# Performance work log

Measured on AMD Instinct MI355X. Metric: run time of the kernel, lower is better.

Reference implementation:

```python
import jax, jax.numpy as jnp
import numpy as np

NEG_SLOPE = 0.2  # PyG GATConv default negative_slope
EPS = 1e-16


def gat_conv(x, src, dst, num_nodes, W, att_src, att_dst, bias, concat):
    """PyG-style GATConv (eval mode, no dropout). att_*: [H, C]."""
    H, C = att_src.shape
    h = (x @ W).reshape(num_nodes, H, C)                      # [N,H,C]
    a_s = jnp.einsum('nhc,hc->nh', h, att_src)                # [N,H]
    a_d = jnp.einsum('nhc,hc->nh', h, att_dst)                # [N,H]
    e = jax.nn.leaky_relu(a_s[src] + a_d[dst], NEG_SLOPE)     # [E,H]
    # segment softmax over edges grouped by destination node
    m = jax.lax.stop_gradient(jax.ops.segment_max(e, dst, num_segments=num_nodes))
    ex = jnp.exp(e - m[dst])
    denom = jax.ops.segment_sum(ex, dst, num_segments=num_nodes)
    alpha = ex / (denom[dst] + EPS)                           # [E,H]
    msg = h[src] * alpha[:, :, None]                          # [E,H,C]
    out = jax.ops.segment_sum(msg, dst, num_segments=num_nodes)  # [N,H,C]
    out = out.reshape(num_nodes, H * C) if concat else out.mean(axis=1)
    return out + bias


def setup_inputs() -> dict:
    key = jax.random.key(0)
    ks = jax.random.split(key, 12)
    N, E = 65536, 1310720
    IN, HID, OUT, HEADS = 768, 128, 2, 8
    C1 = HID // HEADS  # 16
    s = 0.05
    return {
        'x': jax.random.normal(ks[0], (N, IN), jnp.float32),
        'edge_index': jax.random.randint(ks[1], (2, E), 0, N, jnp.int64),
        'W1': jax.random.normal(ks[2], (IN, HEADS * C1), jnp.float32) * s,
        'att_src1': jax.random.normal(ks[3], (HEADS, C1), jnp.float32) * s,
        'att_dst1': jax.random.normal(ks[4], (HEADS, C1), jnp.float32) * s,
        'b1': jnp.zeros((HID,), jnp.float32),
        'Wp': jax.random.normal(ks[5], (IN, HID), jnp.float32) * s,
        'bp': jnp.zeros((HID,), jnp.float32),
        'W2': jax.random.normal(ks[6], (HID, OUT), jnp.float32) * s,
        'att_src2': jax.random.normal(ks[7], (1, OUT), jnp.float32) * s,
        'att_dst2': jax.random.normal(ks[8], (1, OUT), jnp.float32) * s,
        'b2': jnp.zeros((OUT,), jnp.float32),
    }


def reference(x, edge_index, W1, att_src1, att_dst1, b1, Wp, bp, W2, att_src2, att_dst2, b2):
    N = x.shape[0]
    loops = jnp.arange(N, dtype=edge_index.dtype)  # add_self_loops=True
    src = jnp.concatenate([edge_index[0], loops])
    dst = jnp.concatenate([edge_index[1], loops])
    # eval mode: dropout is identity
    h1 = gat_conv(x, src, dst, N, W1, att_src1, att_dst1, b1, concat=True)
    h = jax.nn.elu(h1 + x @ Wp + bp)  # residual projection + ELU
    return gat_conv(h, src, dst, N, W2, att_src2, att_dst2, b2, concat=False)
```

## Files before the change

kernel.cpp:

```cpp
#include <hip/hip_runtime.h>
#include <hip/hip_bf16.h>
#include <math.h>

#define NEG_SLOPE 0.2f

typedef __attribute__((ext_vector_type(8))) short short8;
typedef __attribute__((ext_vector_type(4))) float float4v;

__device__ __forceinline__ unsigned f2bf(float f) {
  unsigned u = __builtin_bit_cast(unsigned, f);
  return (u + 0x7fffu + ((u >> 16) & 1u)) >> 16;
}
__device__ __forceinline__ float bflo(unsigned u) {
  return __builtin_bit_cast(float, u << 16);
}
__device__ __forceinline__ float bfhi(unsigned u) {
  return __builtin_bit_cast(float, u & 0xffff0000u);
}

__global__ __launch_bounds__(256) void convert_w(const float* __restrict__ W1,
                                                 const float* __restrict__ Wp,
                                                 short* __restrict__ Wt) {
  int k = blockIdx.x;
  int c = threadIdx.x;
  float v = (c < 128) ? W1[k * 128 + c] : Wp[k * 128 + (c - 128)];
  Wt[(size_t)c * 768 + k] = (short)f2bf(v);
}

__global__ __launch_bounds__(256) void gemm_mfma(
    const float* __restrict__ x, const short* __restrict__ Wt,
    const float* __restrict__ att_src1, const float* __restrict__ att_dst1,
    float* __restrict__ proj, unsigned* __restrict__ h1bf,
    float* __restrict__ a_s1, float* __restrict__ a_d1) {
  __shared__ short As[128][40];
  __shared__ short Bs[256][40];
  const int tid = threadIdx.x;
  const int wave = tid >> 6, lane = tid & 63;
  const int l15 = lane & 15, l4 = lane >> 4;
  const int row0 = blockIdx.x * 128;

  const int ar = tid >> 3;
  const int ak = (tid & 7) * 4;
  const int bc = tid >> 2;
  const int bk = (tid & 3) * 8;

  float4v acc[8][4] = {};

  for (int k0 = 0; k0 < 768; k0 += 32) {
#pragma unroll
    for (int i = 0; i < 4; i++) {
      int r = i * 32 + ar;
      float4 f = *(const float4*)&x[(size_t)(row0 + r) * 768 + k0 + ak];
      uint2 p;
      p.x = f2bf(f.x) | (f2bf(f.y) << 16);
      p.y = f2bf(f.z) | (f2bf(f.w) << 16);
      *(uint2*)&As[r][ak] = p;
    }
#pragma unroll
    for (int i = 0; i < 4; i++) {
      int c = i * 64 + bc;
      uint4 v = *(const uint4*)&Wt[(size_t)c * 768 + k0 + bk];
      *(uint4*)&Bs[c][bk] = v;
    }
    __syncthreads();

    short8 afr[8];
#pragma unroll
    for (int rt = 0; rt < 8; rt++)
      afr[rt] = *(const short8*)&As[rt * 16 + l15][l4 * 8];
#pragma unroll
    for (int ct = 0; ct < 4; ct++) {
      short8 bfr = *(const short8*)&Bs[wave * 64 + ct * 16 + l15][l4 * 8];
#pragma unroll
      for (int rt = 0; rt < 8; rt++)
        acc[rt][ct] =
            __builtin_amdgcn_mfma_f32_16x16x32_bf16(afr[rt], bfr, acc[rt][ct], 0, 0, 0);
    }
    __syncthreads();
  }

  const int colbase = wave * 64;
  if (wave < 2) {
#pragma unroll
    for (int ct = 0; ct < 4; ct++) {
      const int c = colbase + ct * 16 + l15;
      const int head = wave * 4 + ct;
      const float asw = att_src1[c];
      const float adw = att_dst1[c];
#pragma unroll
      for (int rt = 0; rt < 8; rt++) {
#pragma unroll
        for (int r = 0; r < 4; r++) {
          const int R = row0 + rt * 16 + l4 * 4 + r;
          const float v = acc[rt][ct][r];
          unsigned u = f2bf(v);
          unsigned up = __shfl_xor(u, 1);
          if ((l15 & 1) == 0) h1bf[(size_t)R * 64 + (c >> 1)] = u | (up << 16);
          float as = v * asw, ad = v * adw;
#pragma unroll
          for (int off = 8; off; off >>= 1) {
            as += __shfl_xor(as, off);
            ad += __shfl_xor(ad, off);
          }
          if (l15 == 0) {
            a_s1[R * 8 + head] = as;
            a_d1[R * 8 + head] = ad;
          }
        }
      }
    }
  } else {
#pragma unroll
    for (int ct = 0; ct < 4; ct++) {
      const int c = colbase - 128 + ct * 16 + l15;
#pragma unroll
      for (int rt = 0; rt < 8; rt++) {
#pragma unroll
        for (int r = 0; r < 4; r++) {
          const int R = row0 + rt * 16 + l4 * 4 + r;
          proj[(size_t)R * 128 + c] = acc[rt][ct][r];
        }
      }
    }
  }
}

__global__ void init_counts(int* counts, int N) {
  int i = blockIdx.x * blockDim.x + threadIdx.x;
  if (i < N) counts[i] = 1;
}

__global__ void hist_kernel(const int* __restrict__ dst, int* counts, int E) {
  int i = blockIdx.x * blockDim.x + threadIdx.x;
  int base = i * 4;
  if (base + 3 < E) {
    int4 d = *(const int4*)&dst[base];
    atomicAdd(&counts[d.x], 1);
    atomicAdd(&counts[d.y], 1);
    atomicAdd(&counts[d.z], 1);
    atomicAdd(&counts[d.w], 1);
  } else {
    for (int j = base; j < E; j++) atomicAdd(&counts[dst[j]], 1);
  }
}

__global__ __launch_bounds__(256) void scan_a(const int* __restrict__ counts,
                                              int* offsets, int* bsum) {
  __shared__ int s[256];
  int t = threadIdx.x, idx = blockIdx.x * 256 + t;
  int v = counts[idx];
  s[t] = v;
  __syncthreads();
  for (int d = 1; d < 256; d <<= 1) {
    int x = (t >= d) ? s[t - d] : 0;
    __syncthreads();
    s[t] += x;
    __syncthreads();
  }
  offsets[idx] = s[t] - v;
  if (t == 255) bsum[blockIdx.x] = s[t];
}

__global__ __launch_bounds__(256) void scan_b(int* bsum) {
  __shared__ int s[256];
  int t = threadIdx.x;
  int v = bsum[t];
  s[t] = v;
  __syncthreads();
  for (int d = 1; d < 256; d <<= 1) {
    int x = (t >= d) ? s[t - d] : 0;
    __syncthreads();
    s[t] += x;
    __syncthreads();
  }
  bsum[t] = s[t] - v;
}

__global__ __launch_bounds__(256) void scan_c(int* offsets, const int* bsum,
                                              int* cursor, int* sortedsrc,
                                              int N, int Etot) {
  int t = threadIdx.x, idx = blockIdx.x * 256 + t;
  int off = offsets[idx] + bsum[blockIdx.x];
  offsets[idx] = off;
  sortedsrc[off] = idx;
  cursor[idx] = off + 1;
  if (idx == 0) offsets[N] = Etot;
}

__global__ void scatter_edges(const int* __restrict__ src,
                              const int* __restrict__ dst, int* cursor,
                              int* sortedsrc, int E) {
  int i = blockIdx.x * blockDim.x + threadIdx.x;
  int base = i * 4;
  if (base + 3 < E) {
    int4 s = *(const int4*)&src[base];
    int4 d = *(const int4*)&dst[base];
    sortedsrc[atomicAdd(&cursor[d.x], 1)] = s.x;
    sortedsrc[atomicAdd(&cursor[d.y], 1)] = s.y;
    sortedsrc[atomicAdd(&cursor[d.z], 1)] = s.z;
    sortedsrc[atomicAdd(&cursor[d.w], 1)] = s.w;
  } else {
    for (int j = base; j < E; j++)
      sortedsrc[atomicAdd(&cursor[dst[j]], 1)] = src[j];
  }
}

__global__ __launch_bounds__(256) void agg1_fused(
    const uint4* __restrict__ h1bf4, const float* __restrict__ proj,
    const float* __restrict__ a_s1, const float* __restrict__ a_d1,
    const int* __restrict__ offsets, const int* __restrict__ sortedsrc,
    const float* __restrict__ b1, const float* __restrict__ bp,
    const float* __restrict__ W2, const float* __restrict__ att_s2,
    const float* __restrict__ att_d2, float* __restrict__ h2,
    float* __restrict__ as2, float* __restrict__ ad2) {
  const int t = threadIdx.x;
  const int n = blockIdx.x * 16 + (t >> 4);
  const int k = t & 15;
  const int hd = k >> 1;
  const float ad = a_d1[n * 8 + hd];
  const int begin = offsets[n], end = offsets[n + 1];
  float acc[8] = {};
  float aw = 0.f;
  int j = begin;
  for (; j + 4 <= end; j += 4) {
    int s0 = sortedsrc[j], s1 = sortedsrc[j + 1];
    int s2 = sortedsrc[j + 2], s3 = sortedsrc[j + 3];
    float e0 = a_s1[s0 * 8 + hd], e1 = a_s1[s1 * 8 + hd];
    float e2 = a_s1[s2 * 8 + hd], e3 = a_s1[s3 * 8 + hd];
    uint4 q0 = h1bf4[(size_t)s0 * 16 + k];
    uint4 q1 = h1bf4[(size_t)s1 * 16 + k];
    uint4 q2 = h1bf4[(size_t)s2 * 16 + k];
    uint4 q3 = h1bf4[(size_t)s3 * 16 + k];
    e0 += ad; e1 += ad; e2 += ad; e3 += ad;
    float w0 = __expf(e0 > 0.f ? e0 : NEG_SLOPE * e0);
    float w1 = __expf(e1 > 0.f ? e1 : NEG_SLOPE * e1);
    float w2 = __expf(e2 > 0.f ? e2 : NEG_SLOPE * e2);
    float w3 = __expf(e3 > 0.f ? e3 : NEG_SLOPE * e3);
    acc[0] += w0 * bflo(q0.x) + w1 * bflo(q1.x) + w2 * bflo(q2.x) + w3 * bflo(q3.x);
    acc[1] += w0 * bfhi(q0.x) + w1 * bfhi(q1.x) + w2 * bfhi(q2.x) + w3 * bfhi(q3.x);
    acc[2] += w0 * bflo(q0.y) + w1 * bflo(q1.y) + w2 * bflo(q2.y) + w3 * bflo(q3.y);
    acc[3] += w0 * bfhi(q0.y) + w1 * bfhi(q1.y) + w2 * bfhi(q2.y) + w3 * bfhi(q3.y);
    acc[4] += w0 * bflo(q0.z) + w1 * bflo(q1.z) + w2 * bflo(q2.z) + w3 * bflo(q3.z);
    acc[5] += w0 * bfhi(q0.z) + w1 * bfhi(q1.z) + w2 * bfhi(q2.z) + w3 * bfhi(q3.z);
    acc[6] += w0 * bflo(q0.w) + w1 * bflo(q1.w) + w2 * bflo(q2.w) + w3 * bflo(q3.w);
    acc[7] += w0 * bfhi(q0.w) + w1 * bfhi(q1.w) + w2 * bfhi(q2.w) + w3 * bfhi(q3.w);
    aw += (w0 + w1) + (w2 + w3);
  }
  for (; j < end; j++) {
    int s0 = sortedsrc[j];
    float e0 = a_s1[s0 * 8 + hd] + ad;
    uint4 q0 = h1bf4[(size_t)s0 * 16 + k];
    float w0 = __expf(e0 > 0.f ? e0 : NEG_SLOPE * e0);
    acc[0] += w0 * bflo(q0.x);
    acc[1] += w0 * bfhi(q0.x);
    acc[2] += w0 * bflo(q0.y);
    acc[3] += w0 * bfhi(q0.y);
    acc[4] += w0 * bflo(q0.z);
    acc[5] += w0 * bfhi(q0.z);
    acc[6] += w0 * bflo(q0.w);
    acc[7] += w0 * bfhi(q0.w);
    aw += w0;
  }
  const float inv = 1.f / (aw + 1e-16f);
  const float4 pj0 = *(const float4*)&proj[(size_t)n * 128 + k * 8];
  const float4 pj1 = *(const float4*)&proj[(size_t)n * 128 + k * 8 + 4];
  const float4 b1a = *(const float4*)&b1[k * 8];
  const float4 b1b = *(const float4*)&b1[k * 8 + 4];
  const float4 bpa = *(const float4*)&bp[k * 8];
  const float4 bpb = *(const float4*)&bp[k * 8 + 4];
  float v[8];
  v[0] = acc[0] * inv + pj0.x + b1a.x + bpa.x;
  v[1] = acc[1] * inv + pj0.y + b1a.y + bpa.y;
  v[2] = acc[2] * inv + pj0.z + b1a.z + bpa.z;
  v[3] = acc[3] * inv + pj0.w + b1a.w + bpa.w;
  v[4] = acc[4] * inv + pj1.x + b1b.x + bpb.x;
  v[5] = acc[5] * inv + pj1.y + b1b.y + bpb.y;
  v[6] = acc[6] * inv + pj1.z + b1b.z + bpb.z;
  v[7] = acc[7] * inv + pj1.w + b1b.w + bpb.w;
  float p0 = 0.f, p1 = 0.f;
#pragma unroll
  for (int i = 0; i < 8; i++) {
    float vi = v[i] > 0.f ? v[i] : (__expf(v[i]) - 1.f);
    float2 w2 = *(const float2*)&W2[(k * 8 + i) * 2];
    p0 += vi * w2.x;
    p1 += vi * w2.y;
  }
#pragma unroll
  for (int off = 8; off; off >>= 1) {
    p0 += __shfl_xor(p0, off);
    p1 += __shfl_xor(p1, off);
  }
  if (k == 0) {
    h2[2 * n] = p0;
    h2[2 * n + 1] = p1;
    as2[n] = p0 * att_s2[0] + p1 * att_s2[1];
    ad2[n] = p0 * att_d2[0] + p1 * att_d2[1];
  }
}

__global__ __launch_bounds__(256) void agg2(
    const float* __restrict__ h2, const float* __restrict__ as2,
    const float* __restrict__ ad2, const int* __restrict__ offsets,
    const int* __restrict__ sortedsrc, const float* __restrict__ b2,
    float* __restrict__ out, int N) {
  const int node = blockIdx.x * 16 + (threadIdx.x >> 4);
  const int lane = threadIdx.x & 15;
  const int begin = offsets[node], end = offsets[node + 1];
  const float ad = ad2[node];
  float acc0 = 0.f, acc1 = 0.f, aw = 0.f;
  for (int j = begin + lane; j < end; j += 16) {
    int s = sortedsrc[j];
    float e = as2[s] + ad;
    float w = __expf(e > 0.f ? e : NEG_SLOPE * e);
    float2 hh = *(const float2*)&h2[2 * s];
    acc0 += w * hh.x;
    acc1 += w * hh.y;
    aw += w;
  }
#pragma unroll
  for (int off = 8; off; off >>= 1) {
    acc0 += __shfl_xor(acc0, off);
    acc1 += __shfl_xor(acc1, off);
    aw += __shfl_xor(aw, off);
  }
  if (lane == 0) {
    float inv = 1.f / (aw + 1e-16f);
    out[2 * node] = acc0 * inv + b2[0];
    out[2 * node + 1] = acc1 * inv + b2[1];
  }
}

extern "C" void kernel_launch(void* const* d_in, const int* in_sizes, int n_in,
                              void* d_out, int out_size, void* d_ws,
                              size_t ws_size, hipStream_t stream) {
  const float* x = (const float*)d_in[0];
  const int* edge_index = (const int*)d_in[1];
  const float* W1 = (const float*)d_in[2];
  const float* att_src1 = (const float*)d_in[3];
  const float* att_dst1 = (const float*)d_in[4];
  const float* b1 = (const float*)d_in[5];
  const float* Wp = (const float*)d_in[6];
  const float* bp = (const float*)d_in[7];
  const float* W2 = (const float*)d_in[8];
  const float* att_src2 = (const float*)d_in[9];
  const float* att_dst2 = (const float*)d_in[10];
  const float* b2 = (const float*)d_in[11];
  float* out = (float*)d_out;

  const int N = in_sizes[0] / 768;
  const int E = in_sizes[1] / 2;
  const int Etot = E + N;
  const int* src = edge_index;
  const int* dst = edge_index + E;

  char* ws = (char*)d_ws;
  size_t off = 0;
  auto alloc = [&](size_t bytes) {
    size_t cur = off;
    off += (bytes + 255) & ~(size_t)255;
    return (void*)(ws + cur);
  };
  float* proj = (float*)alloc((size_t)N * 128 * 4);
  unsigned* h1bf = (unsigned*)alloc((size_t)N * 64 * 4);
  float* a_s1 = (float*)alloc((size_t)N * 8 * 4);
  float* a_d1 = (float*)alloc((size_t)N * 8 * 4);
  float* h2 = (float*)alloc((size_t)N * 2 * 4);
  float* as2 = (float*)alloc((size_t)N * 4);
  float* ad2 = (float*)alloc((size_t)N * 4);
  int* counts = (int*)alloc((size_t)N * 4);
  int* offsets = (int*)alloc(((size_t)N + 1) * 4);
  int* cursor = (int*)alloc((size_t)N * 4);
  int* bsum = (int*)alloc(256 * 4);
  int* sortedsrc = (int*)alloc((size_t)Etot * 4);
  short* Wt = (short*)alloc((size_t)256 * 768 * 2);

  convert_w<<<768, 256, 0, stream>>>(W1, Wp, Wt);
  gemm_mfma<<<N / 128, 256, 0, stream>>>(x, Wt, att_src1, att_dst1, proj, h1bf,
                                         a_s1, a_d1);
  init_counts<<<(N + 255) / 256, 256, 0, stream>>>(counts, N);
  hist_kernel<<<(E / 4 + 255) / 256, 256, 0, stream>>>(dst, counts, E);
  scan_a<<<N / 256, 256, 0, stream>>>(counts, offsets, bsum);
  scan_b<<<1, 256, 0, stream>>>(bsum);
  scan_c<<<N / 256, 256, 0, stream>>>(offsets, bsum, cursor, sortedsrc, N,
                                      Etot);
  scatter_edges<<<(E / 4 + 255) / 256, 256, 0, stream>>>(src, dst, cursor,
                                                         sortedsrc, E);
  agg1_fused<<<N / 16, 256, 0, stream>>>((const uint4*)h1bf, proj, a_s1, a_d1,
                                         offsets, sortedsrc, b1, bp, W2,
                                         att_src2, att_dst2, h2, as2, ad2);
  agg2<<<N / 16, 256, 0, stream>>>(h2, as2, ad2, offsets, sortedsrc, b2, out,
                                   N);
}
```

Measured before the change: 612.6 us.

## Halve GEMM row tile and move attention-logit dot products to separate kernel

The GEMM block tile drops from 128 to 64 rows, halving accumulator registers and doubling the grid to 1024 blocks for better occupancy and load balance across CUs. The per-head attention logit reductions (shuffle trees in the epilogue) move out of the GEMM into a new small kernel that reads the bf16 h1 back and computes a_s1/a_d1. This adds an extra launch and an extra read of h1, and the logits are now computed from bf16-rounded h1 rather than fp32 accumulators, which slightly changes numerics. The W tile is now reloaded by twice as many blocks.

```diff
diff --git a/kernel.cpp b/kernel.cpp
--- a/kernel.cpp
+++ b/kernel.cpp
@@ -27,28 +27,27 @@
   Wt[(size_t)c * 768 + k] = (short)f2bf(v);
 }
 
-__global__ __launch_bounds__(256) void gemm_mfma(
-    const float* __restrict__ x, const short* __restrict__ Wt,
-    const float* __restrict__ att_src1, const float* __restrict__ att_dst1,
-    float* __restrict__ proj, unsigned* __restrict__ h1bf,
-    float* __restrict__ a_s1, float* __restrict__ a_d1) {
-  __shared__ short As[128][40];
+__global__ __launch_bounds__(256) void gemm_mfma(const float* __restrict__ x,
+                                                 const short* __restrict__ Wt,
+                                                 float* __restrict__ proj,
+                                                 unsigned* __restrict__ h1bf) {
+  __shared__ short As[64][40];
   __shared__ short Bs[256][40];
   const int tid = threadIdx.x;
   const int wave = tid >> 6, lane = tid & 63;
   const int l15 = lane & 15, l4 = lane >> 4;
-  const int row0 = blockIdx.x * 128;
+  const int row0 = blockIdx.x * 64;
 
   const int ar = tid >> 3;
   const int ak = (tid & 7) * 4;
   const int bc = tid >> 2;
   const int bk = (tid & 3) * 8;
 
-  float4v acc[8][4] = {};
+  float4v acc[4][4] = {};
 
   for (int k0 = 0; k0 < 768; k0 += 32) {
 #pragma unroll
-    for (int i = 0; i < 4; i++) {
+    for (int i = 0; i < 2; i++) {
       int r = i * 32 + ar;
       float4 f = *(const float4*)&x[(size_t)(row0 + r) * 768 + k0 + ak];
       uint2 p;
@@ -64,15 +63,15 @@
     }
     __syncthreads();
 
-    short8 afr[8];
-#pragma unroll
-    for (int rt = 0; rt < 8; rt++)
+    short8 afr[4];
+#pragma unroll
+    for (int rt = 0; rt < 4; rt++)
       afr[rt] = *(const short8*)&As[rt * 16 + l15][l4 * 8];
 #pragma unroll
     for (int ct = 0; ct < 4; ct++) {
       short8 bfr = *(const short8*)&Bs[wave * 64 + ct * 16 + l15][l4 * 8];
 #pragma unroll
-      for (int rt = 0; rt < 8; rt++)
+      for (int rt = 0; rt < 4; rt++)
         acc[rt][ct] =
             __builtin_amdgcn_mfma_f32_16x16x32_bf16(afr[rt], bfr, acc[rt][ct], 0, 0, 0);
     }
@@ -84,28 +83,14 @@
 #pragma unroll
     for (int ct = 0; ct < 4; ct++) {
       const int c = colbase + ct * 16 + l15;
-      const int head = wave * 4 + ct;
-      const float asw = att_src1[c];
-      const float adw = att_dst1[c];
-#pragma unroll
-      for (int rt = 0; rt < 8; rt++) {
+#pragma unroll
+      for (int rt = 0; rt < 4; rt++) {
 #pragma unroll
         for (int r = 0; r < 4; r++) {
           const int R = row0 + rt * 16 + l4 * 4 + r;
-          const float v = acc[rt][ct][r];
-          unsigned u = f2bf(v);
+          unsigned u = f2bf(acc[rt][ct][r]);
           unsigned up = __shfl_xor(u, 1);
           if ((l15 & 1) == 0) h1bf[(size_t)R * 64 + (c >> 1)] = u | (up << 16);
-          float as = v * asw, ad = v * adw;
-#pragma unroll
-          for (int off = 8; off; off >>= 1) {
-            as += __shfl_xor(as, off);
-            ad += __shfl_xor(ad, off);
-          }
-          if (l15 == 0) {
-            a_s1[R * 8 + head] = as;
-            a_d1[R * 8 + head] = ad;
-          }
         }
       }
     }
@@ -114,7 +99,7 @@
     for (int ct = 0; ct < 4; ct++) {
       const int c = colbase - 128 + ct * 16 + l15;
 #pragma unroll
-      for (int rt = 0; rt < 8; rt++) {
+      for (int rt = 0; rt < 4; rt++) {
 #pragma unroll
         for (int r = 0; r < 4; r++) {
           const int R = row0 + rt * 16 + l4 * 4 + r;
@@ -123,6 +108,30 @@
       }
     }
   }
+}
+
+__global__ __launch_bounds__(256) void attn1b(const uint4* __restrict__ h1bf4,
+                                              const float* __restrict__ att_src1,
+                                              const float* __restrict__ att_dst1,
+                                              float* __restrict__ a_s1,
+                                              float* __restrict__ a_d1) {
+  const int t = blockIdx.x * 256 + threadIdx.x;
+  const int n = t >> 3, h = t & 7;
+  uint4 q0 = h1bf4[(size_t)n * 16 + h * 2];
+  uint4 q1 = h1bf4[(size_t)n * 16 + h * 2 + 1];
+  float v[16];
+  v[0] = bflo(q0.x); v[1] = bfhi(q0.x); v[2] = bflo(q0.y); v[3] = bfhi(q0.y);
+  v[4] = bflo(q0.z); v[5] = bfhi(q0.z); v[6] = bflo(q0.w); v[7] = bfhi(q0.w);
+  v[8] = bflo(q1.x); v[9] = bfhi(q1.x); v[10] = bflo(q1.y); v[11] = bfhi(q1.y);
+  v[12] = bflo(q1.z); v[13] = bfhi(q1.z); v[14] = bflo(q1.w); v[15] = bfhi(q1.w);
+  float as = 0.f, ad = 0.f;
+#pragma unroll
+  for (int i = 0; i < 16; i++) {
+    as += v[i] * att_src1[h * 16 + i];
+    ad += v[i] * att_dst1[h * 16 + i];
+  }
+  a_s1[t] = as;
+  a_d1[t] = ad;
 }
 
 __global__ void init_counts(int* counts, int N) {
@@ -375,8 +384,9 @@
   short* Wt = (short*)alloc((size_t)256 * 768 * 2);
 
   convert_w<<<768, 256, 0, stream>>>(W1, Wp, Wt);
-  gemm_mfma<<<N / 128, 256, 0, stream>>>(x, Wt, att_src1, att_dst1, proj, h1bf,
-                                         a_s1, a_d1);
+  gemm_mfma<<<N / 64, 256, 0, stream>>>(x, Wt, proj, h1bf);
+  attn1b<<<N * 8 / 256, 256, 0, stream>>>((const uint4*)h1bf, att_src1,
+                                          att_dst1, a_s1, a_d1);
   init_counts<<<(N + 255) / 256, 256, 0, stream>>>(counts, N);
   hist_kernel<<<(E / 4 + 255) / 256, 256, 0, stream>>>(dst, counts, E);
   scan_a<<<N / 256, 256, 0, stream>>>(counts, offsets, bsum);
```

After: 568.1 us. -7.3%, faster.
